# Kernel tuning notes

Measured on AMD Instinct MI355X. Metric: run time of the kernel, lower is better.

## Reference

```python
import jax, jax.numpy as jnp
import numpy as np

SLOPE = 0.1
EPS = 1e-5


def setup_inputs() -> dict:
    key = jax.random.key(0)
    ks = jax.random.split(key, 12)
    C, INTER, RED = 256, 128, 32
    B, H, W = 8, 128, 128
    s = 0.05
    return {
        "x": jax.random.normal(ks[0], (B, C, H, W), jnp.float32),
        "se_w1": jax.random.normal(ks[1], (RED, C), jnp.float32) * s,
        "se_w2": jax.random.normal(ks[2], (C, RED), jnp.float32) * s,
        "wq": jax.random.normal(ks[3], (INTER, C), jnp.float32) * s,
        "bq": jax.random.normal(ks[4], (INTER,), jnp.float32) * s,
        "wk": jax.random.normal(ks[5], (INTER, C), jnp.float32) * s,
        "bk": jax.random.normal(ks[6], (INTER,), jnp.float32) * s,
        "wv": jax.random.normal(ks[7], (INTER, C), jnp.float32) * s,
        "bv": jax.random.normal(ks[8], (INTER,), jnp.float32) * s,
        "w_wg": jax.random.normal(ks[9], (INTER, INTER), jnp.float32) * s,
        "g_wg": jnp.ones((INTER,), jnp.float32),
        "be_wg": jnp.zeros((INTER,), jnp.float32),
        "rm_wg": jnp.zeros((INTER,), jnp.float32),
        "rv_wg": jnp.ones((INTER,), jnp.float32),
        "w_out": jax.random.normal(ks[10], (C, INTER), jnp.float32) * s,
        "b_out": jax.random.normal(ks[11], (C,), jnp.float32) * s,
        "g_out": jnp.ones((C,), jnp.float32),
        "be_out": jnp.zeros((C,), jnp.float32),
        "rm_out": jnp.zeros((C,), jnp.float32),
        "rv_out": jnp.ones((C,), jnp.float32),
    }


def _bn(x, g, b, rm, rv):
    # eval-mode batch norm over channel axis 1; x: [b, c, ...]
    shape = (1, -1) + (1,) * (x.ndim - 2)
    inv = g / jnp.sqrt(rv + EPS)
    return x * inv.reshape(shape) + (b - rm * inv).reshape(shape)


def reference(x, se_w1, se_w2, wq, bq, wk, bk, wv, bv,
              w_wg, g_wg, be_wg, rm_wg, rv_wg,
              w_out, b_out, g_out, be_out, rm_out, rv_out):
    B, C, H, W = x.shape
    # ---- Speactral_Attention (SE block) ----
    y = x.mean(axis=(2, 3))                                  # [b, c]
    y = jax.nn.leaky_relu(y @ se_w1.T, SLOPE)                # [b, c//8]
    y = jax.nn.sigmoid(y @ se_w2.T)                          # [b, c]
    xs = x * y[:, :, None, None]
    # ---- Spatial_GR ----
    xf = xs.reshape(B, C, H * W)                             # [b, c, n]
    q = jnp.einsum('ic,bcn->bin', wq, xf) + bq[None, :, None]
    k = jnp.einsum('ic,bcn->bin', wk, xf) + bk[None, :, None]
    v = jnp.einsum('ic,bcn->bin', wv, xf) + bv[None, :, None]
    # AV = softmax(q @ v^T) over last dim: [b, i, i]
    att = jax.nn.softmax(jnp.einsum('bin,bjn->bij', q, v), axis=2)
    # bmm(k^T, att) then transpose -> av[b,i,n] = sum_j att[b,j,i] * k[b,j,n]
    av = jnp.einsum('bji,bjn->bin', att, k)                  # [b, inter, n]
    avw = jnp.einsum('oi,bin->bon', w_wg, av)                # conv1d k=1, no bias
    avw = _bn(avw, g_wg, be_wg, rm_wg, rv_wg)
    out = jnp.einsum('co,bon->bcn', w_out, avw) + b_out[None, :, None]
    out = _bn(out.reshape(B, C, H, W), g_out, be_out, rm_out, rv_out)
    return jax.nn.leaky_relu(out + xs, SLOPE)
```

## Files before the change

kernel.cpp:

```cpp
#include <hip/hip_runtime.h>
#include <hip/hip_fp16.h>

#define NPIX 16384
#define CCH 256
#define INTR 128
#define REDD 32
#define NB 8
#define SLOPE 0.1f
#define BNEPS 1e-5f

typedef _Float16 f16x8 __attribute__((ext_vector_type(8)));
typedef __attribute__((ext_vector_type(16))) float f32x16;

#define OFF_GX    0
#define OFF_YM    524288
#define OFF_SC    526336
#define OFF_RS    528384
#define OFF_QS    530432
#define OFF_VS    531456
#define OFF_SWG   532480
#define OFF_TWG   532608
#define OFF_SOUT  532736
#define OFF_TOUT  532992
#define OFF_M     795392
#define OFF_WAV   926464
#define OFF_W2    1188608
#define OFF_W7    1450752
#define OFF_B6    1975040
#define OFF_XH    1977088
#define OFF_PART  18754304

__device__ __forceinline__ unsigned short h1(float f) {
    __half h = __float2half(f);
    return __half_as_ushort(h);
}

__device__ __forceinline__ uint4 cvt8h(const float4 a, const float4 c) {
    __half2 p0 = __floats2half2_rn(a.x, a.y);
    __half2 p1 = __floats2half2_rn(a.z, a.w);
    __half2 p2 = __floats2half2_rn(c.x, c.y);
    __half2 p3 = __floats2half2_rn(c.z, c.w);
    uint4 r;
    r.x = *(unsigned int*)&p0; r.y = *(unsigned int*)&p1;
    r.z = *(unsigned int*)&p2; r.w = *(unsigned int*)&p3;
    return r;
}

__device__ __forceinline__ void gload_lds16(const void* g, void* l) {
    __builtin_amdgcn_global_load_lds((const __attribute__((address_space(1))) void*)g,
                                     (__attribute__((address_space(3))) void*)l, 16, 0, 0);
}

__global__ __launch_bounds__(256) void cvtrow_kernel(const float* __restrict__ x,
                                                     unsigned short* __restrict__ xh,
                                                     float* __restrict__ ymsum) {
    int row = blockIdx.x;
    const float4* p4 = (const float4*)(x + (size_t)row * NPIX);
    uint4* o4 = (uint4*)(xh + (size_t)row * NPIX);
    float s = 0.f;
    for (int i = threadIdx.x; i < NPIX / 8; i += 256) {
        float4 v0 = p4[2 * i];
        float4 v1 = p4[2 * i + 1];
        s += (v0.x + v0.y) + (v0.z + v0.w) + (v1.x + v1.y) + (v1.z + v1.w);
        o4[i] = cvt8h(v0, v1);
    }
    for (int off = 32; off > 0; off >>= 1) s += __shfl_xor(s, off);
    __shared__ float red[4];
    if ((threadIdx.x & 63) == 0) red[threadIdx.x >> 6] = s;
    __syncthreads();
    if (threadIdx.x == 0)
        ymsum[row] = red[0] + red[1] + red[2] + red[3];
}

__global__ __launch_bounds__(256) void se_kernel(const float* __restrict__ ymsum,
                                                 const float* __restrict__ se_w1,
                                                 const float* __restrict__ se_w2,
                                                 float* __restrict__ scale,
                                                 float* __restrict__ rsum) {
    int b = blockIdx.x, t = threadIdx.x;
    __shared__ float ys[CCH];
    __shared__ float y1s[REDD];
    float ymr = ymsum[b * CCH + t];
    ys[t] = ymr * (1.f / 16384.f);
    __syncthreads();
    if (t < REDD) {
        float a = 0.f;
        #pragma unroll 4
        for (int c = 0; c < CCH; ++c) a += se_w1[t * CCH + c] * ys[c];
        y1s[t] = a > 0.f ? a : SLOPE * a;
    }
    __syncthreads();
    float a = 0.f;
    #pragma unroll
    for (int r = 0; r < REDD; ++r) a += se_w2[t * REDD + r] * y1s[r];
    float sg = 1.f / (1.f + expf(-a));
    scale[b * CCH + t] = sg;
    rsum[b * CCH + t] = sg * ymr;
}

__global__ __launch_bounds__(256) void prep_kernel(const float* __restrict__ g_wg, const float* __restrict__ be_wg,
                                                   const float* __restrict__ rm_wg, const float* __restrict__ rv_wg,
                                                   const float* __restrict__ g_out, const float* __restrict__ be_out,
                                                   const float* __restrict__ rm_out, const float* __restrict__ rv_out,
                                                   float* __restrict__ swg, float* __restrict__ twg,
                                                   float* __restrict__ sout, float* __restrict__ tout) {
    int t = threadIdx.x;
    if (t < INTR) {
        float s = g_wg[t] / sqrtf(rv_wg[t] + BNEPS);
        swg[t] = s;
        twg[t] = be_wg[t] - rm_wg[t] * s;
    }
    float s = g_out[t] / sqrtf(rv_out[t] + BNEPS);
    sout[t] = s;
    tout[t] = be_out[t] - rm_out[t] * s;
}

__global__ __launch_bounds__(256) void qsvs_kernel(const float* __restrict__ wq,
                                                   const float* __restrict__ wv,
                                                   const float* __restrict__ rsum,
                                                   float* __restrict__ qs, float* __restrict__ vs) {
    int b = blockIdx.x, t = threadIdx.x;
    __shared__ float rs[CCH];
    rs[t] = rsum[b * CCH + t];
    __syncthreads();
    const float* w = (t < INTR) ? (wq + t * CCH) : (wv + (t - INTR) * CCH);
    float a = 0.f;
    #pragma unroll 4
    for (int c = 0; c < CCH; ++c) a += w[c] * rs[c];
    if (t < INTR) qs[b * INTR + t] = a;
    else          vs[b * INTR + (t - INTR)] = a;
}

__global__ __launch_bounds__(256) void gram_partial_kernel(const unsigned short* __restrict__ xh,
                                                           unsigned short* __restrict__ partials,
                                                           int nch) {
    __shared__ __align__(16) unsigned short Ah[128 * 64];
    __shared__ __align__(16) unsigned short Bh[128 * 64];
    int bid = blockIdx.x;
    int chunk = bid % nch;
    int t2 = bid / nch;
    int tile = t2 % 3;
    int b = t2 / 3;
    int rowbase = (tile == 1) ? 128 : 0;
    int colbase = (tile == 0) ? 0 : 128;
    bool diag = (tile < 2);
    const unsigned short* xb = xh + (size_t)b * CCH * NPIX;
    int kpb = NPIX / nch;
    int n0 = chunk * kpb;
    int nsteps = kpb >> 6;
    int tid = threadIdx.x;
    int l = tid & 63, w = tid >> 6;
    int wrow = (w >> 1) * 64, wcol = (w & 1) * 64;
    int sr = l >> 3, ssg = l & 7;

    f32x16 acc[2][2];
    #pragma unroll
    for (int i = 0; i < 2; ++i)
        #pragma unroll
        for (int j = 0; j < 2; ++j)
            #pragma unroll
            for (int r = 0; r < 16; ++r) acc[i][j][r] = 0.f;

    for (int step = 0; step < nsteps; ++step) {
        int k0 = n0 + step * 64;
        __syncthreads();
        #pragma unroll
        for (int e = 0; e < 4; ++e) {
            int rbase = e * 32 + w * 8;
            int r = rbase + sr;
            int seg = ssg ^ (r & 7);
            gload_lds16(&xb[(size_t)(rowbase + r) * NPIX + k0 + seg * 8], &Ah[rbase * 64]);
            if (!diag)
                gload_lds16(&xb[(size_t)(colbase + r) * NPIX + k0 + seg * 8], &Bh[rbase * 64]);
        }
        __syncthreads();
        const unsigned short* BP = diag ? Ah : Bh;
        #pragma unroll
        for (int kk = 0; kk < 4; ++kk) {
            int useg = kk * 2 + (l >> 5);
            f16x8 af[2], bf[2];
            #pragma unroll
            for (int at = 0; at < 2; ++at) {
                int r = wrow + at * 32 + (l & 31);
                af[at] = *(const f16x8*)&Ah[r * 64 + ((useg ^ (r & 7)) << 3)];
            }
            #pragma unroll
            for (int bt = 0; bt < 2; ++bt) {
                int c = wcol + bt * 32 + (l & 31);
                bf[bt] = *(const f16x8*)&BP[c * 64 + ((useg ^ (c & 7)) << 3)];
            }
            #pragma unroll
            for (int at = 0; at < 2; ++at)
                #pragma unroll
                for (int bt = 0; bt < 2; ++bt)
                    acc[at][bt] = __builtin_amdgcn_mfma_f32_32x32x16_f16(af[at], bf[bt], acc[at][bt], 0, 0, 0);
        }
    }
    unsigned short* P = partials + (size_t)bid * (128 * 128);
    #pragma unroll
    for (int at = 0; at < 2; ++at)
        #pragma unroll
        for (int bt = 0; bt < 2; ++bt)
            #pragma unroll
            for (int r = 0; r < 16; ++r) {
                int lr = wrow + at * 32 + (r & 3) + ((r >> 2) << 3) + ((l >> 5) << 2);
                int lc = wcol + bt * 32 + (l & 31);
                P[lr * 128 + lc] = h1(acc[at][bt][r]);
            }
}

__global__ __launch_bounds__(256) void gram_reduce_kernel(const unsigned short* __restrict__ partials,
                                                          float* __restrict__ Gx,
                                                          int nch) {
    int bid = blockIdx.x;
    int part = bid & 15;
    int tileIdx = bid >> 4;
    int tile = tileIdx % 3;
    int b = tileIdx / 3;
    int rowbase = (tile == 1) ? 128 : 0;
    int colbase = (tile == 0) ? 0 : 128;
    int locIdx = part * 1024 + threadIdx.x * 4;
    const unsigned short* P = partials + (size_t)tileIdx * nch * (128 * 128) + locIdx;
    float4 s = make_float4(0.f, 0.f, 0.f, 0.f);
    for (int ch = 0; ch < nch; ++ch) {
        ushort4 v = *(const ushort4*)(P + (size_t)ch * (128 * 128));
        s.x += __half2float(__ushort_as_half(v.x));
        s.y += __half2float(__ushort_as_half(v.y));
        s.z += __half2float(__ushort_as_half(v.z));
        s.w += __half2float(__ushort_as_half(v.w));
    }
    int lr = locIdx >> 7, lc = locIdx & 127;
    float* G = Gx + (size_t)b * CCH * CCH;
    *(float4*)&G[(rowbase + lr) * CCH + colbase + lc] = s;
    if (tile == 2) {
        G[(colbase + lc + 0) * CCH + rowbase + lr] = s.x;
        G[(colbase + lc + 1) * CCH + rowbase + lr] = s.y;
        G[(colbase + lc + 2) * CCH + rowbase + lr] = s.z;
        G[(colbase + lc + 3) * CCH + rowbase + lr] = s.w;
    }
}

__global__ __launch_bounds__(256) void ts_kernel(const float* __restrict__ wq,
                                                 const float* __restrict__ scale,
                                                 const float* __restrict__ Gx,
                                                 const float* __restrict__ wv,
                                                 const float* __restrict__ bq,
                                                 const float* __restrict__ bv,
                                                 const float* __restrict__ qs,
                                                 const float* __restrict__ vs,
                                                 float* __restrict__ M) {
    int bid = blockIdx.x;
    int i = bid & 127, b = bid >> 7;
    int t = threadIdx.x;
    __shared__ float sw[CCH];
    __shared__ float t1s[CCH];
    __shared__ float part[256];
    __shared__ float redm[2], reds[2];
    sw[t] = wq[i * CCH + t] * scale[b * CCH + t];
    __syncthreads();
    const float* G = Gx + (size_t)b * CCH * CCH;
    float acc = 0.f;
    #pragma unroll 4
    for (int c = 0; c < CCH; ++c) acc += sw[c] * G[c * CCH + t];
    t1s[t] = acc * scale[b * CCH + t];
    __syncthreads();
    int j = t & 127, h = t >> 7;
    const float* wvr = wv + j * CCH + h * 128;
    const float* tp = t1s + h * 128;
    float p = 0.f;
    #pragma unroll 4
    for (int c = 0; c < 128; ++c) p += tp[c] * wvr[c];
    part[t] = p;
    __syncthreads();
    float acc2 = 0.f;
    if (t < 128)
        acc2 = part[t] + part[t + 128]
             + bq[i] * vs[b * INTR + j] + bv[j] * qs[b * INTR + i] + 16384.f * bq[i] * bv[j];
    float m = acc2;
    for (int off = 32; off > 0; off >>= 1) m = fmaxf(m, __shfl_xor(m, off));
    if (t == 0) redm[0] = m;
    if (t == 64) redm[1] = m;
    __syncthreads();
    m = fmaxf(redm[0], redm[1]);
    float e = expf(acc2 - m);
    float s = e;
    for (int off = 32; off > 0; off >>= 1) s += __shfl_xor(s, off);
    if (t == 0) reds[0] = s;
    if (t == 64) reds[1] = s;
    __syncthreads();
    s = reds[0] + reds[1];
    if (t < 128)
        M[(size_t)b * INTR * INTR + j * INTR + i] = e / s;
}

__global__ __launch_bounds__(256) void wav_kernel(const float* __restrict__ M,
                                                  const float* __restrict__ wk,
                                                  float* __restrict__ Wav) {
    int bid = blockIdx.x;
    int i = bid & 127, b = bid >> 7;
    int t = threadIdx.x;
    __shared__ float ms[INTR];
    if (t < INTR) ms[t] = M[(size_t)b * INTR * INTR + i * INTR + t];
    __syncthreads();
    float acc = 0.f;
    #pragma unroll 4
    for (int jj = 0; jj < INTR; ++jj) acc += ms[jj] * wk[jj * CCH + t];
    Wav[(size_t)b * INTR * CCH + i * CCH + t] = acc;
}

__global__ __launch_bounds__(256) void biaschain_kernel(const float* __restrict__ M,
                                                        const float* __restrict__ bk,
                                                        const float* __restrict__ wwg,
                                                        const float* __restrict__ swg,
                                                        const float* __restrict__ twg,
                                                        const float* __restrict__ wout,
                                                        const float* __restrict__ bout,
                                                        const float* __restrict__ sout,
                                                        const float* __restrict__ tout,
                                                        float* __restrict__ b6) {
    int b = blockIdx.x, t = threadIdx.x;
    __shared__ float bavs[INTR], b2s[INTR];
    if (t < INTR) {
        float a = 0.f;
        #pragma unroll 4
        for (int j = 0; j < INTR; ++j) a += M[(size_t)b * INTR * INTR + t * INTR + j] * bk[j];
        bavs[t] = a;
    }
    __syncthreads();
    if (t < INTR) {
        float a = 0.f;
        #pragma unroll 4
        for (int i = 0; i < INTR; ++i) a += wwg[t * INTR + i] * bavs[i];
        b2s[t] = swg[t] * a + twg[t];
    }
    __syncthreads();
    float a = 0.f;
    #pragma unroll 4
    for (int o = 0; o < INTR; ++o) a += wout[t * INTR + o] * b2s[o];
    float b5 = a + bout[t];
    b6[b * CCH + t] = sout[t] * b5 + tout[t];
}

__global__ __launch_bounds__(256) void w2_kernel(const float* __restrict__ wwg,
                                                 const float* __restrict__ Wav,
                                                 const float* __restrict__ swg,
                                                 float* __restrict__ W2) {
    int bid = blockIdx.x;
    int o = bid & 127, b = bid >> 7;
    int t = threadIdx.x;
    __shared__ float wr[INTR];
    if (t < INTR) wr[t] = wwg[o * INTR + t];
    __syncthreads();
    float acc = 0.f;
    #pragma unroll 4
    for (int i = 0; i < INTR; ++i) acc += wr[i] * Wav[(size_t)b * INTR * CCH + i * CCH + t];
    W2[(size_t)b * INTR * CCH + o * CCH + t] = swg[o] * acc;
}

__global__ __launch_bounds__(256) void w7_kernel(const float* __restrict__ wout,
                                                 const float* __restrict__ W2,
                                                 const float* __restrict__ sout,
                                                 const float* __restrict__ scale,
                                                 unsigned short* __restrict__ W7h) {
    int bid = blockIdx.x;
    int c = bid & 255, b = bid >> 8;
    int t = threadIdx.x;
    __shared__ float wr[INTR];
    if (t < INTR) wr[t] = wout[c * INTR + t];
    __syncthreads();
    float acc = 0.f;
    #pragma unroll 4
    for (int o = 0; o < INTR; ++o) acc += wr[o] * W2[(size_t)b * INTR * CCH + o * CCH + t];
    float w6 = sout[c] * acc + ((c == t) ? 1.f : 0.f);
    W7h[(size_t)b * CCH * CCH + c * CCH + t] = h1(w6 * scale[b * CCH + t]);
}

__global__ __launch_bounds__(256, 4) void final_mfma_kernel(const unsigned short* __restrict__ W7h,
                                                            const unsigned short* __restrict__ xh,
                                                            const float* __restrict__ b6,
                                                            float* __restrict__ out) {
    __shared__ __align__(16) unsigned short Ws[128 * 64];
    __shared__ __align__(16) unsigned short Xs[128 * 64];
    int bid0 = blockIdx.x;
    int bid = (bid0 & 7) * 256 + (bid0 >> 3);
    int ct = bid & 1;
    int nt = (bid >> 1) & 127;
    int b = bid >> 8;
    int cbase = ct * 128, n0 = nt * 128;
    const unsigned short* xb = xh + (size_t)b * CCH * NPIX;
    const unsigned short* Wb = W7h + (size_t)b * CCH * CCH;
    int tid = threadIdx.x;
    int l = tid & 63, w = tid >> 6;
    int wrow = (w >> 1) * 64, wcol = (w & 1) * 64;
    int mn = tid & 31, mk0 = tid >> 5;
    int sr = l >> 3, ssg = l & 7;

    f32x16 acc[2][2];
    #pragma unroll
    for (int i = 0; i < 2; ++i)
        #pragma unroll
        for (int j = 0; j < 2; ++j)
            #pragma unroll
            for (int r = 0; r < 16; ++r) acc[i][j][r] = 0.f;

    for (int step = 0; step < 4; ++step) {
        int k0 = step * 64;
        __syncthreads();
        #pragma unroll
        for (int e = 0; e < 4; ++e) {
            int rbase = e * 32 + w * 8;
            int r = rbase + sr;
            int seg = ssg ^ (r & 7);
            gload_lds16(&Wb[(size_t)(cbase + r) * CCH + k0 + seg * 8], &Ws[rbase * 64]);
        }
        #pragma unroll
        for (int mi = 0; mi < 2; ++mi) {
            int mk = mk0 + mi * 8;
            const unsigned short* sp = &xb[(size_t)(k0 + mk * 4) * NPIX + n0 + mn * 4];
            ushort4 q0 = *(const ushort4*)sp;
            ushort4 q1 = *(const ushort4*)(sp + NPIX);
            ushort4 q2 = *(const ushort4*)(sp + 2 * NPIX);
            ushort4 q3 = *(const ushort4*)(sp + 3 * NPIX);
            int klo = mk * 4;
            int unit = klo >> 3, sub = (klo & 7) >> 2;
            #pragma unroll
            for (int j = 0; j < 4; ++j) {
                unsigned short e0 = j == 0 ? q0.x : j == 1 ? q0.y : j == 2 ? q0.z : q0.w;
                unsigned short e1 = j == 0 ? q1.x : j == 1 ? q1.y : j == 2 ? q1.z : q1.w;
                unsigned short e2 = j == 0 ? q2.x : j == 1 ? q2.y : j == 2 ? q2.z : q2.w;
                unsigned short e3 = j == 0 ? q3.x : j == 1 ? q3.y : j == 2 ? q3.z : q3.w;
                int nl = mn * 4 + j;
                ushort4 cv = make_ushort4(e0, e1, e2, e3);
                int idx = nl * 64 + ((unit ^ ((nl >> 2) & 7)) << 3) + sub * 4;
                *(ushort4*)&Xs[idx] = cv;
            }
        }
        __syncthreads();
        #pragma unroll
        for (int kk = 0; kk < 4; ++kk) {
            int useg = kk * 2 + (l >> 5);
            f16x8 af[2], bfr[2];
            #pragma unroll
            for (int at = 0; at < 2; ++at) {
                int c = wrow + at * 32 + (l & 31);
                af[at] = *(const f16x8*)&Ws[c * 64 + ((useg ^ (c & 7)) << 3)];
            }
            #pragma unroll
            for (int bt = 0; bt < 2; ++bt) {
                int n = wcol + bt * 32 + (l & 31);
                bfr[bt] = *(const f16x8*)&Xs[n * 64 + ((useg ^ ((n >> 2) & 7)) << 3)];
            }
            #pragma unroll
            for (int at = 0; at < 2; ++at)
                #pragma unroll
                for (int bt = 0; bt < 2; ++bt)
                    acc[at][bt] = __builtin_amdgcn_mfma_f32_32x32x16_f16(af[at], bfr[bt], acc[at][bt], 0, 0, 0);
        }
    }
    #pragma unroll
    for (int at = 0; at < 2; ++at)
        #pragma unroll
        for (int bt = 0; bt < 2; ++bt)
            #pragma unroll
            for (int r = 0; r < 16; ++r) {
                int c = cbase + wrow + at * 32 + (r & 3) + ((r >> 2) << 3) + ((l >> 5) << 2);
                int n = n0 + wcol + bt * 32 + (l & 31);
                float v = acc[at][bt][r] + b6[b * CCH + c];
                v = v > 0.f ? v : SLOPE * v;
                out[(size_t)b * CCH * NPIX + (size_t)c * NPIX + n] = v;
            }
}

extern "C" void kernel_launch(void* const* d_in, const int* in_sizes, int n_in,
                              void* d_out, int out_size, void* d_ws, size_t ws_size,
                              hipStream_t stream) {
    (void)in_sizes; (void)n_in; (void)out_size;
    const float* x      = (const float*)d_in[0];
    const float* se_w1  = (const float*)d_in[1];
    const float* se_w2  = (const float*)d_in[2];
    const float* wq     = (const float*)d_in[3];
    const float* bq     = (const float*)d_in[4];
    const float* wk     = (const float*)d_in[5];
    const float* bk     = (const float*)d_in[6];
    const float* wv     = (const float*)d_in[7];
    const float* bv     = (const float*)d_in[8];
    const float* w_wg   = (const float*)d_in[9];
    const float* w_out  = (const float*)d_in[14];
    const float* b_out  = (const float*)d_in[15];
    float* out = (float*)d_out;
    float* ws = (float*)d_ws;
    unsigned short* xh = (unsigned short*)(ws + OFF_XH);

    size_t avail = ws_size / sizeof(float);
    int nch = 32;
    while (nch > 1 && (size_t)OFF_PART + (size_t)NB * 3 * nch * 8192 > avail) nch >>= 1;

    cvtrow_kernel<<<NB * CCH, 256, 0, stream>>>(x, xh, ws + OFF_YM);
    gram_partial_kernel<<<NB * 3 * nch, 256, 0, stream>>>(xh, (unsigned short*)(ws + OFF_PART), nch);
    gram_reduce_kernel<<<NB * 3 * 16, 256, 0, stream>>>((const unsigned short*)(ws + OFF_PART),
                                                        ws + OFF_GX, nch);
    se_kernel<<<NB, 256, 0, stream>>>(ws + OFF_YM, se_w1, se_w2, ws + OFF_SC, ws + OFF_RS);
    prep_kernel<<<1, 256, 0, stream>>>((const float*)d_in[10], (const float*)d_in[11],
                                       (const float*)d_in[12], (const float*)d_in[13],
                                       (const float*)d_in[16], (const float*)d_in[17],
                                       (const float*)d_in[18], (const float*)d_in[19],
                                       ws + OFF_SWG, ws + OFF_TWG, ws + OFF_SOUT, ws + OFF_TOUT);
    qsvs_kernel<<<NB, 256, 0, stream>>>(wq, wv, ws + OFF_RS, ws + OFF_QS, ws + OFF_VS);
    ts_kernel<<<NB * INTR, 256, 0, stream>>>(wq, ws + OFF_SC, ws + OFF_GX, wv, bq, bv,
                                             ws + OFF_QS, ws + OFF_VS, ws + OFF_M);
    wav_kernel<<<NB * INTR, 256, 0, stream>>>(ws + OFF_M, wk, ws + OFF_WAV);
    biaschain_kernel<<<NB, 256, 0, stream>>>(ws + OFF_M, bk, w_wg, ws + OFF_SWG, ws + OFF_TWG,
                                             w_out, b_out, ws + OFF_SOUT, ws + OFF_TOUT, ws + OFF_B6);
    w2_kernel<<<NB * INTR, 256, 0, stream>>>(w_wg, ws + OFF_WAV, ws + OFF_SWG, ws + OFF_W2);
    w7_kernel<<<NB * CCH, 256, 0, stream>>>(w_out, ws + OFF_W2, ws + OFF_SOUT, ws + OFF_SC,
                                            (unsigned short*)(ws + OFF_W7));
    final_mfma_kernel<<<NB * 2 * 128, 256, 0, stream>>>((const unsigned short*)(ws + OFF_W7),
                                                        xh, ws + OFF_B6, out);
}
```

Baseline: 238.4 us.

## Fuse small weight-chain kernels into head and MFMA-based tail kernels

Merges the SE, BN-prep and q/v-sum kernels into one head kernel. It also replaces the four weight-chain kernels (wav, biaschain, w2, w7) with a single per-batch tail kernel that does the three chained 128/256 matrix products with fp16 MFMA through swizzled LDS tiles. The aim is to remove several launches and the global round trips of the Wav and W2 intermediates. The cost is that the tail runs on only 8 blocks, so it is serialised per batch with low occupancy, and the intermediates are now rounded to fp16, which may reduce accuracy.

```diff
diff --git a/kernel.cpp b/kernel.cpp
--- a/kernel.cpp
+++ b/kernel.cpp
@@ -15,7 +15,6 @@
 #define OFF_GX    0
 #define OFF_YM    524288
 #define OFF_SC    526336
-#define OFF_RS    528384
 #define OFF_QS    530432
 #define OFF_VS    531456
 #define OFF_SWG   532480
@@ -23,8 +22,6 @@
 #define OFF_SOUT  532736
 #define OFF_TOUT  532992
 #define OFF_M     795392
-#define OFF_WAV   926464
-#define OFF_W2    1188608
 #define OFF_W7    1450752
 #define OFF_B6    1975040
 #define OFF_XH    1977088
@@ -44,6 +41,11 @@
     r.x = *(unsigned int*)&p0; r.y = *(unsigned int*)&p1;
     r.z = *(unsigned int*)&p2; r.w = *(unsigned int*)&p3;
     return r;
+}
+
+__device__ __forceinline__ f16x8 cvt8hf(const float4 a, const float4 c) {
+    uint4 u = cvt8h(a, c);
+    return *(f16x8*)&u;
 }
 
 __device__ __forceinline__ void gload_lds16(const void* g, void* l) {
@@ -72,16 +74,33 @@
         ymsum[row] = red[0] + red[1] + red[2] + red[3];
 }
 
-__global__ __launch_bounds__(256) void se_kernel(const float* __restrict__ ymsum,
-                                                 const float* __restrict__ se_w1,
-                                                 const float* __restrict__ se_w2,
-                                                 float* __restrict__ scale,
-                                                 float* __restrict__ rsum) {
+__global__ __launch_bounds__(256) void head_kernel(const float* __restrict__ ymsum,
+                                                   const float* __restrict__ se_w1,
+                                                   const float* __restrict__ se_w2,
+                                                   const float* __restrict__ wq,
+                                                   const float* __restrict__ wv,
+                                                   const float* __restrict__ g_wg, const float* __restrict__ be_wg,
+                                                   const float* __restrict__ rm_wg, const float* __restrict__ rv_wg,
+                                                   const float* __restrict__ g_out, const float* __restrict__ be_out,
+                                                   const float* __restrict__ rm_out, const float* __restrict__ rv_out,
+                                                   float* __restrict__ scale,
+                                                   float* __restrict__ qs, float* __restrict__ vs,
+                                                   float* __restrict__ swg, float* __restrict__ twg,
+                                                   float* __restrict__ sout, float* __restrict__ tout) {
     int b = blockIdx.x, t = threadIdx.x;
-    __shared__ float ys[CCH];
-    __shared__ float y1s[REDD];
+    __shared__ float ys[CCH], y1s[REDD], rs[CCH];
     float ymr = ymsum[b * CCH + t];
     ys[t] = ymr * (1.f / 16384.f);
+    if (b == 0) {
+        if (t < INTR) {
+            float s = g_wg[t] / sqrtf(rv_wg[t] + BNEPS);
+            swg[t] = s;
+            twg[t] = be_wg[t] - rm_wg[t] * s;
+        }
+        float s = g_out[t] / sqrtf(rv_out[t] + BNEPS);
+        sout[t] = s;
+        tout[t] = be_out[t] - rm_out[t] * s;
+    }
     __syncthreads();
     if (t < REDD) {
         float a = 0.f;
@@ -95,40 +114,14 @@
     for (int r = 0; r < REDD; ++r) a += se_w2[t * REDD + r] * y1s[r];
     float sg = 1.f / (1.f + expf(-a));
     scale[b * CCH + t] = sg;
-    rsum[b * CCH + t] = sg * ymr;
-}
-
-__global__ __launch_bounds__(256) void prep_kernel(const float* __restrict__ g_wg, const float* __restrict__ be_wg,
-                                                   const float* __restrict__ rm_wg, const float* __restrict__ rv_wg,
-                                                   const float* __restrict__ g_out, const float* __restrict__ be_out,
-                                                   const float* __restrict__ rm_out, const float* __restrict__ rv_out,
-                                                   float* __restrict__ swg, float* __restrict__ twg,
-                                                   float* __restrict__ sout, float* __restrict__ tout) {
-    int t = threadIdx.x;
-    if (t < INTR) {
-        float s = g_wg[t] / sqrtf(rv_wg[t] + BNEPS);
-        swg[t] = s;
-        twg[t] = be_wg[t] - rm_wg[t] * s;
-    }
-    float s = g_out[t] / sqrtf(rv_out[t] + BNEPS);
-    sout[t] = s;
-    tout[t] = be_out[t] - rm_out[t] * s;
-}
-
-__global__ __launch_bounds__(256) void qsvs_kernel(const float* __restrict__ wq,
-                                                   const float* __restrict__ wv,
-                                                   const float* __restrict__ rsum,
-                                                   float* __restrict__ qs, float* __restrict__ vs) {
-    int b = blockIdx.x, t = threadIdx.x;
-    __shared__ float rs[CCH];
-    rs[t] = rsum[b * CCH + t];
+    rs[t] = sg * ymr;
     __syncthreads();
     const float* w = (t < INTR) ? (wq + t * CCH) : (wv + (t - INTR) * CCH);
-    float a = 0.f;
+    float a2 = 0.f;
     #pragma unroll 4
-    for (int c = 0; c < CCH; ++c) a += w[c] * rs[c];
-    if (t < INTR) qs[b * INTR + t] = a;
-    else          vs[b * INTR + (t - INTR)] = a;
+    for (int c = 0; c < CCH; ++c) a2 += w[c] * rs[c];
+    if (t < INTR) qs[b * INTR + t] = a2;
+    else          vs[b * INTR + (t - INTR)] = a2;
 }
 
 __global__ __launch_bounds__(256) void gram_partial_kernel(const unsigned short* __restrict__ xh,
@@ -293,86 +286,201 @@
         M[(size_t)b * INTR * INTR + j * INTR + i] = e / s;
 }
 
-__global__ __launch_bounds__(256) void wav_kernel(const float* __restrict__ M,
-                                                  const float* __restrict__ wk,
-                                                  float* __restrict__ Wav) {
-    int bid = blockIdx.x;
-    int i = bid & 127, b = bid >> 7;
-    int t = threadIdx.x;
-    __shared__ float ms[INTR];
-    if (t < INTR) ms[t] = M[(size_t)b * INTR * INTR + i * INTR + t];
-    __syncthreads();
-    float acc = 0.f;
-    #pragma unroll 4
-    for (int jj = 0; jj < INTR; ++jj) acc += ms[jj] * wk[jj * CCH + t];
-    Wav[(size_t)b * INTR * CCH + i * CCH + t] = acc;
-}
-
-__global__ __launch_bounds__(256) void biaschain_kernel(const float* __restrict__ M,
-                                                        const float* __restrict__ bk,
-                                                        const float* __restrict__ wwg,
-                                                        const float* __restrict__ swg,
-                                                        const float* __restrict__ twg,
-                                                        const float* __restrict__ wout,
-                                                        const float* __restrict__ bout,
-                                                        const float* __restrict__ sout,
-                                                        const float* __restrict__ tout,
-                                                        float* __restrict__ b6) {
-    int b = blockIdx.x, t = threadIdx.x;
-    __shared__ float bavs[INTR], b2s[INTR];
-    if (t < INTR) {
+__global__ __launch_bounds__(256) void tail_kernel(const float* __restrict__ M,
+                                                   const float* __restrict__ wk,
+                                                   const float* __restrict__ bk,
+                                                   const float* __restrict__ wwg,
+                                                   const float* __restrict__ swg,
+                                                   const float* __restrict__ twg,
+                                                   const float* __restrict__ wout,
+                                                   const float* __restrict__ bout,
+                                                   const float* __restrict__ sout,
+                                                   const float* __restrict__ tout,
+                                                   const float* __restrict__ scale,
+                                                   unsigned short* __restrict__ W7h,
+                                                   float* __restrict__ b6) {
+    __shared__ __align__(16) unsigned short Bt[256 * 128];
+    __shared__ __align__(16) unsigned short Ot[256 * 128];
+    __shared__ float bavS[INTR], b2S[INTR], scS[CCH], soS[CCH], swgS[INTR];
+    int b = blockIdx.x, tid = threadIdx.x;
+    int l = tid & 63, w = tid >> 6;
+    const float* Mb = M + (size_t)b * INTR * INTR;
+
+    scS[tid] = scale[b * CCH + tid];
+    soS[tid] = sout[tid];
+    if (tid < INTR) swgS[tid] = swg[tid];
+
+    {
+        int mn = tid & 63;
+        int mk0 = tid >> 6;
+        #pragma unroll
+        for (int e = 0; e < 8; ++e) {
+            int j0 = (mk0 + 4 * e) * 4;
+            int c0 = mn * 4;
+            float4 q0 = *(const float4*)&wk[(size_t)(j0 + 0) * CCH + c0];
+            float4 q1 = *(const float4*)&wk[(size_t)(j0 + 1) * CCH + c0];
+            float4 q2 = *(const float4*)&wk[(size_t)(j0 + 2) * CCH + c0];
+            float4 q3 = *(const float4*)&wk[(size_t)(j0 + 3) * CCH + c0];
+            int unit = j0 >> 3, sub = (j0 >> 2) & 1;
+            int key = (c0 >> 2) & 7;
+            #pragma unroll
+            for (int jj = 0; jj < 4; ++jj) {
+                float e0 = jj == 0 ? q0.x : jj == 1 ? q0.y : jj == 2 ? q0.z : q0.w;
+                float e1 = jj == 0 ? q1.x : jj == 1 ? q1.y : jj == 2 ? q1.z : q1.w;
+                float e2 = jj == 0 ? q2.x : jj == 1 ? q2.y : jj == 2 ? q2.z : q2.w;
+                float e3 = jj == 0 ? q3.x : jj == 1 ? q3.y : jj == 2 ? q3.z : q3.w;
+                ushort4 cv = make_ushort4(h1(e0), h1(e1), h1(e2), h1(e3));
+                *(ushort4*)&Bt[(c0 + jj) * 128 + ((unit ^ key) << 3) + sub * 4] = cv;
+            }
+        }
+    }
+    if (tid < INTR) {
         float a = 0.f;
         #pragma unroll 4
-        for (int j = 0; j < INTR; ++j) a += M[(size_t)b * INTR * INTR + t * INTR + j] * bk[j];
-        bavs[t] = a;
-    }
-    __syncthreads();
-    if (t < INTR) {
-        float a = 0.f;
-        #pragma unroll 4
-        for (int i = 0; i < INTR; ++i) a += wwg[t * INTR + i] * bavs[i];
-        b2s[t] = swg[t] * a + twg[t];
-    }
-    __syncthreads();
-    float a = 0.f;
-    #pragma unroll 4
-    for (int o = 0; o < INTR; ++o) a += wout[t * INTR + o] * b2s[o];
-    float b5 = a + bout[t];
-    b6[b * CCH + t] = sout[t] * b5 + tout[t];
-}
-
-__global__ __launch_bounds__(256) void w2_kernel(const float* __restrict__ wwg,
-                                                 const float* __restrict__ Wav,
-                                                 const float* __restrict__ swg,
-                                                 float* __restrict__ W2) {
-    int bid = blockIdx.x;
-    int o = bid & 127, b = bid >> 7;
-    int t = threadIdx.x;
-    __shared__ float wr[INTR];
-    if (t < INTR) wr[t] = wwg[o * INTR + t];
-    __syncthreads();
-    float acc = 0.f;
-    #pragma unroll 4
-    for (int i = 0; i < INTR; ++i) acc += wr[i] * Wav[(size_t)b * INTR * CCH + i * CCH + t];
-    W2[(size_t)b * INTR * CCH + o * CCH + t] = swg[o] * acc;
-}
-
-__global__ __launch_bounds__(256) void w7_kernel(const float* __restrict__ wout,
-                                                 const float* __restrict__ W2,
-                                                 const float* __restrict__ sout,
-                                                 const float* __restrict__ scale,
-                                                 unsigned short* __restrict__ W7h) {
-    int bid = blockIdx.x;
-    int c = bid & 255, b = bid >> 8;
-    int t = threadIdx.x;
-    __shared__ float wr[INTR];
-    if (t < INTR) wr[t] = wout[c * INTR + t];
-    __syncthreads();
-    float acc = 0.f;
-    #pragma unroll 4
-    for (int o = 0; o < INTR; ++o) acc += wr[o] * W2[(size_t)b * INTR * CCH + o * CCH + t];
-    float w6 = sout[c] * acc + ((c == t) ? 1.f : 0.f);
-    W7h[(size_t)b * CCH * CCH + c * CCH + t] = h1(w6 * scale[b * CCH + t]);
+        for (int j = 0; j < INTR; ++j) a += Mb[tid * INTR + j] * bk[j];
+        bavS[tid] = a;
+    }
+    __syncthreads();
+
+    {
+        f32x16 acc[4][2];
+        #pragma unroll
+        for (int at = 0; at < 4; ++at)
+            #pragma unroll
+            for (int bt = 0; bt < 2; ++bt)
+                #pragma unroll
+                for (int r = 0; r < 16; ++r) acc[at][bt][r] = 0.f;
+        #pragma unroll
+        for (int kk = 0; kk < 8; ++kk) {
+            int useg = kk * 2 + (l >> 5);
+            f16x8 bf[2];
+            #pragma unroll
+            for (int bt = 0; bt < 2; ++bt) {
+                int c = w * 64 + bt * 32 + (l & 31);
+                bf[bt] = *(const f16x8*)&Bt[c * 128 + ((useg ^ ((c >> 2) & 7)) << 3)];
+            }
+            #pragma unroll
+            for (int at = 0; at < 4; ++at) {
+                int i = at * 32 + (l & 31);
+                float4 a0 = *(const float4*)&Mb[(size_t)i * INTR + useg * 8];
+                float4 a1 = *(const float4*)&Mb[(size_t)i * INTR + useg * 8 + 4];
+                f16x8 af = cvt8hf(a0, a1);
+                #pragma unroll
+                for (int bt = 0; bt < 2; ++bt)
+                    acc[at][bt] = __builtin_amdgcn_mfma_f32_32x32x16_f16(af, bf[bt], acc[at][bt], 0, 0, 0);
+            }
+        }
+        if (tid < INTR) {
+            float a = 0.f;
+            #pragma unroll 4
+            for (int i = 0; i < INTR; ++i) a += wwg[tid * INTR + i] * bavS[i];
+            b2S[tid] = swgS[tid] * a + twg[tid];
+        }
+        __syncthreads();
+        #pragma unroll
+        for (int at = 0; at < 4; ++at)
+            #pragma unroll
+            for (int bt = 0; bt < 2; ++bt)
+                #pragma unroll
+                for (int r = 0; r < 16; ++r) {
+                    int i = at * 32 + (r & 3) + ((r >> 2) << 3) + ((l >> 5) << 2);
+                    int c = w * 64 + bt * 32 + (l & 31);
+                    Ot[c * 128 + (((i >> 3) ^ ((c >> 2) & 7)) << 3) + (i & 7)] = h1(acc[at][bt][r]);
+                }
+    }
+    __syncthreads();
+
+    {
+        f32x16 acc[4][2];
+        #pragma unroll
+        for (int at = 0; at < 4; ++at)
+            #pragma unroll
+            for (int bt = 0; bt < 2; ++bt)
+                #pragma unroll
+                for (int r = 0; r < 16; ++r) acc[at][bt][r] = 0.f;
+        #pragma unroll
+        for (int kk = 0; kk < 8; ++kk) {
+            int useg = kk * 2 + (l >> 5);
+            f16x8 bf[2];
+            #pragma unroll
+            for (int bt = 0; bt < 2; ++bt) {
+                int c = w * 64 + bt * 32 + (l & 31);
+                bf[bt] = *(const f16x8*)&Ot[c * 128 + ((useg ^ ((c >> 2) & 7)) << 3)];
+            }
+            #pragma unroll
+            for (int at = 0; at < 4; ++at) {
+                int o = at * 32 + (l & 31);
+                float4 a0 = *(const float4*)&wwg[(size_t)o * INTR + useg * 8];
+                float4 a1 = *(const float4*)&wwg[(size_t)o * INTR + useg * 8 + 4];
+                f16x8 af = cvt8hf(a0, a1);
+                #pragma unroll
+                for (int bt = 0; bt < 2; ++bt)
+                    acc[at][bt] = __builtin_amdgcn_mfma_f32_32x32x16_f16(af, bf[bt], acc[at][bt], 0, 0, 0);
+            }
+        }
+        {
+            float a = 0.f;
+            #pragma unroll 4
+            for (int o = 0; o < INTR; ++o) a += wout[tid * INTR + o] * b2S[o];
+            float b5 = a + bout[tid];
+            b6[b * CCH + tid] = soS[tid] * b5 + tout[tid];
+        }
+        __syncthreads();
+        #pragma unroll
+        for (int at = 0; at < 4; ++at)
+            #pragma unroll
+            for (int bt = 0; bt < 2; ++bt)
+                #pragma unroll
+                for (int r = 0; r < 16; ++r) {
+                    int o = at * 32 + (r & 3) + ((r >> 2) << 3) + ((l >> 5) << 2);
+                    int c = w * 64 + bt * 32 + (l & 31);
+                    Bt[c * 128 + (((o >> 3) ^ ((c >> 2) & 7)) << 3) + (o & 7)] = h1(swgS[o] * acc[at][bt][r]);
+                }
+    }
+    __syncthreads();
+
+    unsigned short* Wb = W7h + (size_t)b * CCH * CCH;
+    #pragma unroll
+    for (int p = 0; p < 2; ++p) {
+        f32x16 acc[4][2];
+        #pragma unroll
+        for (int at = 0; at < 4; ++at)
+            #pragma unroll
+            for (int bt = 0; bt < 2; ++bt)
+                #pragma unroll
+                for (int r = 0; r < 16; ++r) acc[at][bt][r] = 0.f;
+        #pragma unroll
+        for (int kk = 0; kk < 8; ++kk) {
+            int useg = kk * 2 + (l >> 5);
+            f16x8 bf[2];
+            #pragma unroll
+            for (int bt = 0; bt < 2; ++bt) {
+                int cp = w * 64 + bt * 32 + (l & 31);
+                bf[bt] = *(const f16x8*)&Bt[cp * 128 + ((useg ^ ((cp >> 2) & 7)) << 3)];
+            }
+            #pragma unroll
+            for (int at = 0; at < 4; ++at) {
+                int cc = p * 128 + at * 32 + (l & 31);
+                float4 a0 = *(const float4*)&wout[(size_t)cc * INTR + useg * 8];
+                float4 a1 = *(const float4*)&wout[(size_t)cc * INTR + useg * 8 + 4];
+                f16x8 af = cvt8hf(a0, a1);
+                #pragma unroll
+                for (int bt = 0; bt < 2; ++bt)
+                    acc[at][bt] = __builtin_amdgcn_mfma_f32_32x32x16_f16(af, bf[bt], acc[at][bt], 0, 0, 0);
+            }
+        }
+        #pragma unroll
+        for (int at = 0; at < 4; ++at)
+            #pragma unroll
+            for (int bt = 0; bt < 2; ++bt)
+                #pragma unroll
+                for (int r = 0; r < 16; ++r) {
+                    int c = p * 128 + at * 32 + (r & 3) + ((r >> 2) << 3) + ((l >> 5) << 2);
+                    int cp = w * 64 + bt * 32 + (l & 31);
+                    float w6 = soS[c] * acc[at][bt][r] + ((c == cp) ? 1.f : 0.f);
+                    Wb[c * CCH + cp] = h1(w6 * scS[cp]);
+                }
+    }
 }
 
 __global__ __launch_bounds__(256, 4) void final_mfma_kernel(const unsigned short* __restrict__ W7h,
@@ -499,21 +607,18 @@
     gram_partial_kernel<<<NB * 3 * nch, 256, 0, stream>>>(xh, (unsigned short*)(ws + OFF_PART), nch);
     gram_reduce_kernel<<<NB * 3 * 16, 256, 0, stream>>>((const unsigned short*)(ws + OFF_PART),
                                                         ws + OFF_GX, nch);
-    se_kernel<<<NB, 256, 0, stream>>>(ws + OFF_YM, se_w1, se_w2, ws + OFF_SC, ws + OFF_RS);
-    prep_kernel<<<1, 256, 0, stream>>>((const float*)d_in[10], (const float*)d_in[11],
-                                       (const float*)d_in[12], (const float*)d_in[13],
-                                       (const float*)d_in[16], (const float*)d_in[17],
-                                       (const float*)d_in[18], (const float*)d_in[19],
-                                       ws + OFF_SWG, ws + OFF_TWG, ws + OFF_SOUT, ws + OFF_TOUT);
-    qsvs_kernel<<<NB, 256, 0, stream>>>(wq, wv, ws + OFF_RS, ws + OFF_QS, ws + OFF_VS);
+    head_kernel<<<NB, 256, 0, stream>>>(ws + OFF_YM, se_w1, se_w2, wq, wv,
+                                        (const float*)d_in[10], (const float*)d_in[11],
+                                        (const float*)d_in[12], (const float*)d_in[13],
+                                        (const float*)d_in[16], (const float*)d_in[17],
+                                        (const float*)d_in[18], (const float*)d_in[19],
+                                        ws + OFF_SC, ws + OFF_QS, ws + OFF_VS,
+                                        ws + OFF_SWG, ws + OFF_TWG, ws + OFF_SOUT, ws + OFF_TOUT);
     ts_kernel<<<NB * INTR, 256, 0, stream>>>(wq, ws + OFF_SC, ws + OFF_GX, wv, bq, bv,
                                              ws + OFF_QS, ws + OFF_VS, ws + OFF_M);
-    wav_kernel<<<NB * INTR, 256, 0, stream>>>(ws + OFF_M, wk, ws + OFF_WAV);
-    biaschain_kernel<<<NB, 256, 0, stream>>>(ws + OFF_M, bk, w_wg, ws + OFF_SWG, ws + OFF_TWG,
-                                             w_out, b_out, ws + OFF_SOUT, ws + OFF_TOUT, ws + OFF_B6);
-    w2_kernel<<<NB * INTR, 256, 0, stream>>>(w_wg, ws + OFF_WAV, ws + OFF_SWG, ws + OFF_W2);
-    w7_kernel<<<NB * CCH, 256, 0, stream>>>(w_out, ws + OFF_W2, ws + OFF_SOUT, ws + OFF_SC,
-                                            (unsigned short*)(ws + OFF_W7));
+    tail_kernel<<<NB, 256, 0, stream>>>(ws + OFF_M, wk, bk, w_wg, ws + OFF_SWG, ws + OFF_TWG,
+                                        w_out, b_out, ws + OFF_SOUT, ws + OFF_TOUT, ws + OFF_SC,
+                                        (unsigned short*)(ws + OFF_W7), ws + OFF_B6);
     final_mfma_kernel<<<NB * 2 * 128, 256, 0, stream>>>((const unsigned short*)(ws + OFF_W7),
                                                         xh, ws + OFF_B6, out);
 }
```

New measurement: 234.3 us. No clear change (-1.7%).
